# Kernel optimization log

Hardware: AMD Instinct MI355X
Metric: run time of the kernel (lower is better)

The kernel has to match this reference:

```python
import jax, jax.numpy as jnp
import numpy as np

B, N, H, E, WF = 2048, 30, 256, 256, 32
TANH_C = 10.0  # tanh_exploration


def _mask_modify(m):
    # if a row is all True, un-mask the last column
    all_true = jnp.all(m, axis=1)
    return m.at[:, -1].set(m[:, -1] & ~all_true)


def _lstm_cell(x, h, c, W_ih, W_hh, b_ih, b_hh):
    gates = x @ W_ih.T + b_ih + h @ W_hh.T + b_hh
    i, f, g, o = jnp.split(gates, 4, axis=1)  # torch LSTMCell gate order
    c_new = jax.nn.sigmoid(f) * c + jax.nn.sigmoid(i) * jnp.tanh(g)
    h_new = jax.nn.sigmoid(o) * jnp.tanh(c_new)
    return h_new, c_new


def _attention(query, ref, Wq, bq, Wr, br, v, C=None):
    # query [B,H], ref [B,H,N] (context permuted)
    q = query @ Wq.T + bq                                        # [B,H]
    e = jnp.einsum('oh,bhn->bon', Wr, ref) + br[None, :, None]   # 1x1 conv
    u = jnp.einsum('h,bhn->bn', v, jnp.tanh(q[:, :, None] + e))  # [B,N]
    logits = C * jnp.tanh(u) if C is not None else u
    return e, logits


def setup_inputs() -> dict:
    key = jax.random.key(0)
    ks = jax.random.split(key, 24)
    s = 0.06  # ~1/sqrt(H) init scale
    n = lambda k, sh: jax.random.normal(k, sh, dtype=jnp.float32)
    return {
        'decoder_input': n(ks[0], (B, E)),
        'embedded_inputs': n(ks[1], (N, B, E)),
        'h0': n(ks[2], (B, H)),
        'c0': n(ks[3], (B, H)),
        'context': n(ks[4], (N, B, H)),
        'embed_cou': n(ks[5], (B, WF)),
        'D': jax.random.uniform(ks[6], (B, N, N), dtype=jnp.float32),
        'W_ih': n(ks[7], (4 * H, E)) * s,
        'W_hh': n(ks[8], (4 * H, H)) * s,
        'b_ih': n(ks[9], (4 * H,)) * s,
        'b_hh': n(ks[10], (4 * H,)) * s,
        'W_merge': n(ks[11], (H, H + WF)) * s,
        'b_merge': n(ks[12], (H,)) * s,
        'Wq_p': n(ks[13], (H, H)) * s,
        'bq_p': n(ks[14], (H,)) * s,
        'Wr_p': n(ks[15], (H, H)) * s,
        'br_p': n(ks[16], (H,)) * s,
        'v_p': n(ks[17], (H,)) * s,
        'Wq_g': n(ks[18], (H, H)) * s,
        'bq_g': n(ks[19], (H,)) * s,
        'Wr_g': n(ks[20], (H, H)) * s,
        'br_g': n(ks[21], (H,)) * s,
        'v_g': n(ks[22], (H,)) * s,
        'V_reach_mask_t': jnp.zeros((B, N), dtype=bool),
        'start_idx': jax.random.randint(ks[23], (B,), 0, N),
        'k_min_nodes': 3,
    }


def reference(decoder_input, embedded_inputs, h0, c0, context, embed_cou, D,
              W_ih, W_hh, b_ih, b_hh, W_merge, b_merge,
              Wq_p, bq_p, Wr_p, br_p, v_p,
              Wq_g, bq_g, Wr_g, br_g, v_g,
              V_reach_mask_t, start_idx, k_min_nodes):
    ref = jnp.transpose(context, (1, 2, 0))  # [B,H,N]
    arangeB = jnp.arange(B)
    arangeN = jnp.arange(N)

    def step(carry, _):
        h, c, mask, idxs, dec_in, knn_row = carry
        # --- update_knn_mask ('n-1'): builds the row used at the NEXT step ---
        Eb = D[arangeB, idxs]                                  # [B,N]
        weighted = Eb * (~mask).astype(Eb.dtype)
        valid = jnp.sum(~mask, axis=1) > k_min_nodes
        far = jnp.argmax(weighted, axis=1)
        next_row = (arangeN[None, :] == far[:, None]) & valid[:, None]
        # --- recurrence: update_mask + check_mask ---
        lm = mask.at[arangeB, idxs].set(True)
        lm = _mask_modify(_mask_modify(lm))
        full_mask = lm | knn_row
        # LSTM step + worker-feature merge
        hy, cy = _lstm_cell(dec_in, h, c, W_ih, W_hh, b_ih, b_hh)
        g_l = jnp.concatenate([hy, embed_cou], axis=1) @ W_merge.T + b_merge
        # one glimpse (n_glimpses=1)
        e_g, lg = _attention(g_l, ref, Wq_g, bq_g, Wr_g, br_g, v_g)
        lg = jnp.where(full_mask, -jnp.inf, lg)
        g_l = jnp.einsum('bhn,bn->bh', e_g, jax.nn.softmax(lg, axis=1))
        # pointer (use_tanh with C)
        _, lp = _attention(g_l, ref, Wq_p, bq_p, Wr_p, br_p, v_p, C=TANH_C)
        lp = jnp.where(full_mask, -jnp.inf, lp)
        log_p = jax.nn.log_softmax(lp, axis=1)
        new_idxs = jnp.argmax(log_p, axis=1)  # greedy decode
        new_dec = embedded_inputs[new_idxs, arangeB]  # [B,E]
        return (hy, cy, lm, new_idxs, new_dec, next_row), (log_p, new_idxs)

    init = (h0, c0, V_reach_mask_t, start_idx, decoder_input,
            jnp.zeros_like(V_reach_mask_t))
    (_, _, mask, _, _, _), (logps, sels) = jax.lax.scan(step, init, None, length=N)
    return jnp.swapaxes(logps, 0, 1), jnp.swapaxes(sels, 0, 1), mask
```

## Files before the change

### kernel.cpp

```cpp
#include <hip/hip_runtime.h>
#include <hip/hip_bf16.h>
#include <math.h>

#define B 2048
#define NN 30
#define H 256
#define EDIM 256
#define G4 1024
#define PAD 44

typedef __attribute__((ext_vector_type(8))) short short8;
typedef __attribute__((ext_vector_type(4))) float f32x4;

__device__ __forceinline__ float fsig(float x) {
    return __fdividef(1.f, 1.f + __expf(-x));
}
__device__ __forceinline__ float ftanh(float x) {
    return 1.f - __fdividef(2.f, __expf(2.f * x) + 1.f);
}

__device__ __forceinline__ void split3(float a, unsigned short& h,
                                       unsigned short& m_, unsigned short& l_)
{
    unsigned ab = __float_as_uint(a);
    h = (unsigned short)(ab >> 16);
    float r1 = a - __uint_as_float(ab & 0xffff0000u);
    unsigned rb = __float_as_uint(r1);
    m_ = (unsigned short)(rb >> 16);
    float r2 = r1 - __uint_as_float(rb & 0xffff0000u);
    l_ = (unsigned short)(__float_as_uint(r2) >> 16);
}

__global__ __launch_bounds__(256)
void gemm_big(const float* __restrict__ A,
              const unsigned short* __restrict__ Wh, const unsigned short* __restrict__ Wm,
              const unsigned short* __restrict__ Wl,
              const float* __restrict__ b0, const float* __restrict__ b1,
              const float* __restrict__ b2,
              float* __restrict__ C0, float* __restrict__ C1,
              float* __restrict__ C2)
{
    __shared__ __align__(16) unsigned short Ah[128][PAD];
    __shared__ __align__(16) unsigned short Am[128][PAD];
    __shared__ __align__(16) unsigned short Al[128][PAD];
    __shared__ __align__(16) unsigned short Bh[128][PAD];
    __shared__ __align__(16) unsigned short Bm[128][PAD];
    __shared__ __align__(16) unsigned short Bl[128][PAD];

    int tid = threadIdx.x;
    int w = tid >> 6, l = tid & 63;

    int lin = blockIdx.y * 6 + blockIdx.x;
    int v = (lin & 7) * 360 + (lin >> 3);
    int m0 = (v / 6) << 7;
    int nblk = v % 6;
    int part = nblk >> 1;
    int nin = (nblk & 1) << 7;
    const float* bias = part == 0 ? b0 : part == 1 ? b1 : b2;
    float* C          = part == 0 ? C0 : part == 1 ? C1 : C2;
    long woff = (long)part * 65536;

    int srow = tid >> 1;
    int skb  = (tid & 1) << 4;
    const float* arow = A + (long)(m0 + srow) * 256 + skb;
    const unsigned short* wph = Wh + woff + (long)(nin + srow) * 256 + skb;
    const unsigned short* wpm = Wm + woff + (long)(nin + srow) * 256 + skb;
    const unsigned short* wpl = Wl + woff + (long)(nin + srow) * 256 + skb;

    int fr = l & 15;
    int fk = (l >> 4) << 3;

    f32x4 acc[2][8];
    #pragma unroll
    for (int i = 0; i < 2; ++i)
        #pragma unroll
        for (int j = 0; j < 8; ++j)
            acc[i][j] = (f32x4){0.f, 0.f, 0.f, 0.f};

    for (int kt = 0; kt < 8; ++kt) {
        int k0 = kt << 5;
        float4 a4[4];
        #pragma unroll
        for (int i = 0; i < 4; ++i)
            a4[i] = *(const float4*)(arow + k0 + (i << 2));
        short8 wh0 = *(const short8*)(wph + k0);
        short8 wh1 = *(const short8*)(wph + k0 + 8);
        short8 wm0 = *(const short8*)(wpm + k0);
        short8 wm1 = *(const short8*)(wpm + k0 + 8);
        short8 wl0 = *(const short8*)(wpl + k0);
        short8 wl1 = *(const short8*)(wpl + k0 + 8);

        unsigned short th[16], tm[16], tl[16];
        #pragma unroll
        for (int i = 0; i < 4; ++i) {
            float va[4] = {a4[i].x, a4[i].y, a4[i].z, a4[i].w};
            #pragma unroll
            for (int j = 0; j < 4; ++j)
                split3(va[j], th[(i << 2) + j], tm[(i << 2) + j], tl[(i << 2) + j]);
        }

        __syncthreads();
        *(short8*)&Ah[srow][skb]     = *(const short8*)&th[0];
        *(short8*)&Ah[srow][skb + 8] = *(const short8*)&th[8];
        *(short8*)&Am[srow][skb]     = *(const short8*)&tm[0];
        *(short8*)&Am[srow][skb + 8] = *(const short8*)&tm[8];
        *(short8*)&Al[srow][skb]     = *(const short8*)&tl[0];
        *(short8*)&Al[srow][skb + 8] = *(const short8*)&tl[8];
        *(short8*)&Bh[srow][skb]     = wh0;
        *(short8*)&Bh[srow][skb + 8] = wh1;
        *(short8*)&Bm[srow][skb]     = wm0;
        *(short8*)&Bm[srow][skb + 8] = wm1;
        *(short8*)&Bl[srow][skb]     = wl0;
        *(short8*)&Bl[srow][skb + 8] = wl1;
        __syncthreads();

        short8 aH[2], aM[2], aL[2];
        #pragma unroll
        for (int ms = 0; ms < 2; ++ms) {
            int r = (w << 5) + (ms << 4) + fr;
            aH[ms] = *(const short8*)&Ah[r][fk];
            aM[ms] = *(const short8*)&Am[r][fk];
            aL[ms] = *(const short8*)&Al[r][fk];
        }
        #pragma unroll
        for (int ng = 0; ng < 2; ++ng) {
            short8 bH[4], bM[4], bL[4];
            #pragma unroll
            for (int j = 0; j < 4; ++j) {
                int r = (((ng << 2) + j) << 4) + fr;
                bH[j] = *(const short8*)&Bh[r][fk];
                bM[j] = *(const short8*)&Bm[r][fk];
                bL[j] = *(const short8*)&Bl[r][fk];
            }
            #pragma unroll
            for (int ms = 0; ms < 2; ++ms)
                #pragma unroll
                for (int j = 0; j < 4; ++j)
                    acc[ms][(ng << 2) + j] = __builtin_amdgcn_mfma_f32_16x16x32_bf16(
                        aH[ms], bH[j], acc[ms][(ng << 2) + j], 0, 0, 0);
            #pragma unroll
            for (int ms = 0; ms < 2; ++ms)
                #pragma unroll
                for (int j = 0; j < 4; ++j)
                    acc[ms][(ng << 2) + j] = __builtin_amdgcn_mfma_f32_16x16x32_bf16(
                        aH[ms], bM[j], acc[ms][(ng << 2) + j], 0, 0, 0);
            #pragma unroll
            for (int ms = 0; ms < 2; ++ms)
                #pragma unroll
                for (int j = 0; j < 4; ++j)
                    acc[ms][(ng << 2) + j] = __builtin_amdgcn_mfma_f32_16x16x32_bf16(
                        aM[ms], bH[j], acc[ms][(ng << 2) + j], 0, 0, 0);
            #pragma unroll
            for (int ms = 0; ms < 2; ++ms)
                #pragma unroll
                for (int j = 0; j < 4; ++j)
                    acc[ms][(ng << 2) + j] = __builtin_amdgcn_mfma_f32_16x16x32_bf16(
                        aH[ms], bL[j], acc[ms][(ng << 2) + j], 0, 0, 0);
            #pragma unroll
            for (int ms = 0; ms < 2; ++ms)
                #pragma unroll
                for (int j = 0; j < 4; ++j)
                    acc[ms][(ng << 2) + j] = __builtin_amdgcn_mfma_f32_16x16x32_bf16(
                        aM[ms], bM[j], acc[ms][(ng << 2) + j], 0, 0, 0);
            #pragma unroll
            for (int ms = 0; ms < 2; ++ms)
                #pragma unroll
                for (int j = 0; j < 4; ++j)
                    acc[ms][(ng << 2) + j] = __builtin_amdgcn_mfma_f32_16x16x32_bf16(
                        aL[ms], bH[j], acc[ms][(ng << 2) + j], 0, 0, 0);
        }
    }

    #pragma unroll
    for (int ms = 0; ms < 2; ++ms) {
        #pragma unroll
        for (int ns = 0; ns < 8; ++ns) {
            float bv = bias[nin + (ns << 4) + fr];
            #pragma unroll
            for (int r = 0; r < 4; ++r) {
                int m = m0 + (w << 5) + (ms << 4) + ((l >> 4) << 2) + r;
                C[(long)m * 256 + nin + (ns << 4) + fr] = acc[ms][ns][r] + bv;
            }
        }
    }
}

__global__ __launch_bounds__(256)
void gates_mfma(const unsigned short* __restrict__ dhi, const unsigned short* __restrict__ dlo,
                const unsigned short* __restrict__ hhi, const unsigned short* __restrict__ hlo,
                const unsigned short* __restrict__ Whi, const unsigned short* __restrict__ Wlo,
                const float* __restrict__ bsum, const float* __restrict__ cin,
                float* __restrict__ hout, float* __restrict__ cout,
                unsigned short* __restrict__ hohi, unsigned short* __restrict__ holo)
{
    __shared__ __align__(16) unsigned short Ah[128][PAD];
    __shared__ __align__(16) unsigned short Al[128][PAD];
    __shared__ __align__(16) unsigned short Bh[64][PAD];
    __shared__ __align__(16) unsigned short Bl[64][PAD];

    int tid = threadIdx.x;
    int w = tid >> 6, l = tid & 63;
    int lin = blockIdx.x;
    int v = (lin & 7) * 32 + (lin >> 3);
    int m0 = (v >> 4) << 7;
    int u0 = (v & 15) << 4;

    int arow = tid >> 1;
    int akb  = (tid & 1) << 4;
    int brw  = tid >> 2;
    int bkb  = (tid & 3) << 3;
    int wrow = ((brw >> 4) << 8) + u0 + (brw & 15);
    const unsigned short* wph = Whi + (long)wrow * 512 + bkb;
    const unsigned short* wpl = Wlo + (long)wrow * 512 + bkb;

    int fk = (l >> 4) << 3;
    int fr = l & 15;

    f32x4 acc[2][4];
    #pragma unroll
    for (int i = 0; i < 2; ++i)
        #pragma unroll
        for (int j = 0; j < 4; ++j)
            acc[i][j] = (f32x4){0.f, 0.f, 0.f, 0.f};

    for (int kt = 0; kt < 16; ++kt) {
        int k0 = kt << 5;
        const unsigned short* sah; const unsigned short* sal; int kk;
        if (k0 < 256) { sah = dhi; sal = dlo; kk = k0; }
        else          { sah = hhi; sal = hlo; kk = k0 - 256; }
        long abase = (long)(m0 + arow) * 256 + kk + akb;
        short8 a0 = *(const short8*)&sah[abase];
        short8 a1 = *(const short8*)&sah[abase + 8];
        short8 a2 = *(const short8*)&sal[abase];
        short8 a3 = *(const short8*)&sal[abase + 8];
        short8 b0 = *(const short8*)&wph[k0];
        short8 b1 = *(const short8*)&wpl[k0];
        __syncthreads();
        *(short8*)&Ah[arow][akb]     = a0;
        *(short8*)&Ah[arow][akb + 8] = a1;
        *(short8*)&Al[arow][akb]     = a2;
        *(short8*)&Al[arow][akb + 8] = a3;
        *(short8*)&Bh[brw][bkb] = b0;
        *(short8*)&Bl[brw][bkb] = b1;
        __syncthreads();

        short8 aH[2], aL[2], bH[4], bL[4];
        #pragma unroll
        for (int ms = 0; ms < 2; ++ms) {
            int r = (w << 5) + (ms << 4) + fr;
            aH[ms] = *(const short8*)&Ah[r][fk];
            aL[ms] = *(const short8*)&Al[r][fk];
        }
        #pragma unroll
        for (int s = 0; s < 4; ++s) {
            int r = (s << 4) + fr;
            bH[s] = *(const short8*)&Bh[r][fk];
            bL[s] = *(const short8*)&Bl[r][fk];
        }
        #pragma unroll
        for (int ms = 0; ms < 2; ++ms)
            #pragma unroll
            for (int s = 0; s < 4; ++s)
                acc[ms][s] = __builtin_amdgcn_mfma_f32_16x16x32_bf16(aH[ms], bH[s], acc[ms][s], 0, 0, 0);
        #pragma unroll
        for (int ms = 0; ms < 2; ++ms)
            #pragma unroll
            for (int s = 0; s < 4; ++s)
                acc[ms][s] = __builtin_amdgcn_mfma_f32_16x16x32_bf16(aH[ms], bL[s], acc[ms][s], 0, 0, 0);
        #pragma unroll
        for (int ms = 0; ms < 2; ++ms)
            #pragma unroll
            for (int s = 0; s < 4; ++s)
                acc[ms][s] = __builtin_amdgcn_mfma_f32_16x16x32_bf16(aL[ms], bH[s], acc[ms][s], 0, 0, 0);
    }

    int u = u0 + fr;
    float bI = bsum[u], bF = bsum[256 + u], bG = bsum[512 + u], bO = bsum[768 + u];
    #pragma unroll
    for (int ms = 0; ms < 2; ++ms) {
        #pragma unroll
        for (int r = 0; r < 4; ++r) {
            int m = m0 + (w << 5) + (ms << 4) + ((l >> 4) << 2) + r;
            float gi = acc[ms][0][r] + bI;
            float gf = acc[ms][1][r] + bF;
            float gg = acc[ms][2][r] + bG;
            float go = acc[ms][3][r] + bO;
            float cv = cin[(long)m * H + u];
            float cn = fsig(gf) * cv + fsig(gi) * ftanh(gg);
            float hn = fsig(go) * ftanh(cn);
            cout[(long)m * H + u] = cn;
            hout[(long)m * H + u] = hn;
            unsigned hb = __float_as_uint(hn);
            hohi[(long)m * H + u] = (unsigned short)(hb >> 16);
            float lo = hn - __uint_as_float(hb & 0xffff0000u);
            holo[(long)m * H + u] = (unsigned short)(__float_as_uint(lo) >> 16);
        }
    }
}

__global__ void init_state(const unsigned char* __restrict__ vr, const int* __restrict__ start,
                           unsigned char* __restrict__ mask, unsigned char* __restrict__ knn,
                           int* __restrict__ idxs)
{
    int t = blockIdx.x * 256 + threadIdx.x;
    if (t < B * NN) { mask[t] = vr[t] ? 1 : 0; knn[t] = 0; }
    if (t < B) idxs[t] = start[t];
}

__global__ void prep_wsplit(const float* __restrict__ Wih, const float* __restrict__ Whh,
                            const float* __restrict__ bih, const float* __restrict__ bhh,
                            unsigned short* __restrict__ Whi, unsigned short* __restrict__ Wlo,
                            float* __restrict__ bsum)
{
    int n = blockIdx.x, k = threadIdx.x;
    float a = Wih[(long)n * H + k];
    unsigned ab = __float_as_uint(a);
    Whi[(long)n * 512 + k] = (unsigned short)(ab >> 16);
    float alo = a - __uint_as_float(ab & 0xffff0000u);
    Wlo[(long)n * 512 + k] = (unsigned short)(__float_as_uint(alo) >> 16);
    float b = Whh[(long)n * H + k];
    unsigned bb = __float_as_uint(b);
    Whi[(long)n * 512 + 256 + k] = (unsigned short)(bb >> 16);
    float blo = b - __uint_as_float(bb & 0xffff0000u);
    Wlo[(long)n * 512 + 256 + k] = (unsigned short)(__float_as_uint(blo) >> 16);
    if (k == 0) bsum[n] = bih[n] + bhh[n];
}

__global__ void prep_splitW(const float* __restrict__ W0, const float* __restrict__ W1,
                            const float* __restrict__ W2,
                            unsigned short* __restrict__ Wh, unsigned short* __restrict__ Wm,
                            unsigned short* __restrict__ Wl)
{
    int id = blockIdx.x;
    int p = id >> 8, r = id & 255, k = threadIdx.x;
    const float* W = p == 0 ? W0 : p == 1 ? W1 : W2;
    float a = W[(long)r * 256 + k];
    long o = (long)p * 65536 + (long)r * 256 + k;
    split3(a, Wh[o], Wm[o], Wl[o]);
}

__global__ void conv_pair(const float* __restrict__ x,
                          unsigned short* __restrict__ xhi, unsigned short* __restrict__ xlo)
{
    int t = blockIdx.x * 256 + threadIdx.x;
    float a = x[t];
    unsigned ab = __float_as_uint(a);
    xhi[t] = (unsigned short)(ab >> 16);
    float lo = a - __uint_as_float(ab & 0xffff0000u);
    xlo[t] = (unsigned short)(__float_as_uint(lo) >> 16);
}

__global__ void prep_compose1(const float* __restrict__ Wqg, const float* __restrict__ Wm,
                              float* __restrict__ W1cT)
{
    int h = blockIdx.x, k = threadIdx.x;
    float a = 0.f;
    for (int j = 0; j < H; ++j) a = fmaf(Wqg[(long)h * H + j], Wm[(long)j * 288 + k], a);
    W1cT[(long)k * H + h] = a;
}

__global__ void prep_compose2(const float* __restrict__ Wqg, const float* __restrict__ Wm,
                              const float* __restrict__ bm, const float* __restrict__ bqg,
                              float* __restrict__ W2c, float* __restrict__ bc)
{
    int h = blockIdx.x, w = threadIdx.x;
    if (w < 32) {
        float a = 0.f;
        for (int j = 0; j < H; ++j) a = fmaf(Wqg[(long)h * H + j], Wm[(long)j * 288 + 256 + w], a);
        W2c[h * 32 + w] = a;
    } else if (w == 32) {
        float a = 0.f;
        for (int j = 0; j < H; ++j) a = fmaf(Wqg[(long)h * H + j], bm[j], a);
        bc[h] = a + bqg[h];
    }
}

__global__ __launch_bounds__(256)
void prep_qc(const float* __restrict__ cou, const float* __restrict__ W2c,
             const float* __restrict__ bc, float* __restrict__ qc)
{
    __shared__ float sWT[32 * 256];
    __shared__ float sb[256];
    int b = blockIdx.x, h = threadIdx.x;
    for (int i = h; i < 32 * 256; i += 256) {
        int hh = i >> 5, ww = i & 31;
        sWT[ww * 256 + hh] = W2c[i];
    }
    sb[h] = bc[h];
    __syncthreads();
    const float* cr = cou + (long)b * 32;
    float a = sb[h];
    for (int w = 0; w < 32; ++w) a = fmaf(cr[w], sWT[w * 256 + h], a);
    qc[(long)b * H + h] = a;
}

__global__ void prep_composeF(const float* __restrict__ Wqp, const float* __restrict__ Wrg,
                              const float* __restrict__ brg, float* __restrict__ WFc,
                              float* __restrict__ bFc)
{
    int f = blockIdx.x, k = threadIdx.x;
    float a = 0.f;
    for (int j = 0; j < H; ++j) a = fmaf(Wqp[(long)f * H + j], Wrg[(long)j * H + k], a);
    WFc[(long)f * H + k] = a;
    if (k == 0) {
        float s = 0.f;
        for (int j = 0; j < H; ++j) s = fmaf(Wqp[(long)f * H + j], brg[j], s);
        bFc[f] = s;
    }
}

__global__ __launch_bounds__(512)
void mega8(const float* __restrict__ eg, const float* __restrict__ ep,
           const float* __restrict__ F, const float* __restrict__ hout,
           const float* __restrict__ qc, const float* __restrict__ W1cT,
           const float* __restrict__ vg, const float* __restrict__ vp,
           const float* __restrict__ bqp,
           const float* __restrict__ D, const int* __restrict__ kminp,
           unsigned char* __restrict__ mask, unsigned char* __restrict__ knn,
           const float* __restrict__ emb,
           float* __restrict__ out, int step,
           int* __restrict__ idxs,
           unsigned short* __restrict__ dechi, unsigned short* __restrict__ declo)
{
    __shared__ float sHy[4][256];
    __shared__ float sQg[4][256];
    __shared__ float sU[4][32];
    __shared__ float sPar[4][2][256];
    __shared__ unsigned char sFull[4][32];

    int tid = threadIdx.x;
    int wv = tid >> 6, lane = tid & 63;
    int pi = wv >> 1, sub = wv & 1;
    int blk = blockIdx.x;
    int vB = (blk & 7) * 64 + (blk >> 3);
    int b0 = vB << 2;
    int b = b0 + pi;

    #pragma unroll
    for (int i = 0; i < 2; ++i) {
        int idx2 = tid + (i << 9);
        int bl = idx2 >> 8, hh = idx2 & 255;
        sHy[bl][hh] = hout[(long)(b0 + bl) * H + hh];
    }
    __syncthreads();

    {
        int hh = tid & 255, g = tid >> 8;
        float a0 = 0.f, a1 = 0.f;
        const float* wp = W1cT + hh;
        const float* h0p = sHy[(g << 1)];
        const float* h1p = sHy[(g << 1) + 1];
        #pragma unroll 4
        for (int k = 0; k < 256; ++k) {
            float wval = wp[(long)k * H];
            a0 = fmaf(h0p[k], wval, a0);
            a1 = fmaf(h1p[k], wval, a1);
        }
        sQg[(g << 1)][hh]     = qc[(long)(b0 + (g << 1)) * H + hh] + a0;
        sQg[(g << 1) + 1][hh] = qc[(long)(b0 + (g << 1) + 1) * H + hh] + a1;
    }

    if (sub == 0) {
        bool in = lane < NN;
        int idx = idxs[b];
        int kmin = *kminp;
        unsigned char m = in ? mask[b * NN + lane] : (unsigned char)1;
        float dv = in ? D[((long)b * NN + idx) * NN + lane] : 0.f;
        unsigned long long unm = __ballot(in && !m);
        int cnt = __popcll(unm);
        bool valid = cnt > kmin;
        float bw = (in && !m) ? dv : (in ? 0.f : -1.f);
        int bi = in ? lane : 1000;
        #pragma unroll
        for (int off = 32; off; off >>= 1) {
            float ow = __shfl_down(bw, off, 64);
            int oi = __shfl_down(bi, off, 64);
            if (ow > bw || (ow == bw && oi < bi)) { bw = ow; bi = oi; }
        }
        int far = __shfl(bi, 0, 64);
        unsigned char mnew = (in && lane == idx) ? 1 : m;
        #pragma unroll
        for (int rep = 0; rep < 2; ++rep) {
            bool allm = (__ballot(in && !mnew) == 0ull);
            if (allm && lane == NN - 1) mnew = 0;
        }
        unsigned char kn = in ? knn[b * NN + lane] : 0;
        if (in) {
            sFull[pi][lane] = (mnew | kn) ? 1 : 0;
            mask[b * NN + lane] = mnew;
            knn[b * NN + lane] = (lane == far && valid) ? 1 : 0;
        }
    }
    __syncthreads();

    float4 vg4 = ((const float4*)vg)[lane];
    float4 vp4 = ((const float4*)vp)[lane];

    {
        float4 q4 = ((const float4*)&sQg[pi][0])[lane];
        for (int n = sub; n < NN; n += 2) {
            if (sFull[pi][n]) continue;
            float4 e4 = ((const float4*)(eg + ((long)n * B + b) * H))[lane];
            float s = vg4.x * ftanh(q4.x + e4.x);
            s = fmaf(vg4.y, ftanh(q4.y + e4.y), s);
            s = fmaf(vg4.z, ftanh(q4.z + e4.z), s);
            s = fmaf(vg4.w, ftanh(q4.w + e4.w), s);
            #pragma unroll
            for (int off = 32; off; off >>= 1) s += __shfl_down(s, off, 64);
            if (lane == 0) sU[pi][n] = s;
        }
    }
    __syncthreads();

    float pr;
    {
        bool in = lane < NN;
        bool fm = in ? (sFull[pi][lane] != 0) : true;
        float u = (in && !fm) ? sU[pi][lane] : -INFINITY;
        float mx = u;
        #pragma unroll
        for (int off = 32; off; off >>= 1) mx = fmaxf(mx, __shfl_down(mx, off, 64));
        mx = __shfl(mx, 0, 64);
        float p = (in && !fm) ? __expf(u - mx) : 0.f;
        float sum = p;
        #pragma unroll
        for (int off = 32; off; off >>= 1) sum += __shfl_down(sum, off, 64);
        sum = __shfl(sum, 0, 64);
        pr = p / sum;
    }

    {
        float4 qa = {0.f, 0.f, 0.f, 0.f};
        for (int n = sub; n < NN; n += 2) {
            float pn = __shfl(pr, n, 64);
            if (pn != 0.f) {
                float4 F4 = ((const float4*)(F + ((long)n * B + b) * H))[lane];
                qa.x = fmaf(pn, F4.x, qa.x);
                qa.y = fmaf(pn, F4.y, qa.y);
                qa.z = fmaf(pn, F4.z, qa.z);
                qa.w = fmaf(pn, F4.w, qa.w);
            }
        }
        ((float4*)&sPar[pi][sub][0])[lane] = qa;
    }
    __syncthreads();

    float4 qp4;
    {
        float4 p0 = ((const float4*)&sPar[pi][0][0])[lane];
        float4 p1 = ((const float4*)&sPar[pi][1][0])[lane];
        float4 bq4 = ((const float4*)bqp)[lane];
        qp4 = make_float4(bq4.x + p0.x + p1.x, bq4.y + p0.y + p1.y,
                          bq4.z + p0.z + p1.z, bq4.w + p0.w + p1.w);
    }

    for (int n = sub; n < NN; n += 2) {
        if (sFull[pi][n]) continue;
        float4 e4 = ((const float4*)(ep + ((long)n * B + b) * H))[lane];
        float s = vp4.x * ftanh(qp4.x + e4.x);
        s = fmaf(vp4.y, ftanh(qp4.y + e4.y), s);
        s = fmaf(vp4.z, ftanh(qp4.z + e4.z), s);
        s = fmaf(vp4.w, ftanh(qp4.w + e4.w), s);
        #pragma unroll
        for (int off = 32; off; off >>= 1) s += __shfl_down(s, off, 64);
        if (lane == 0) sU[pi][n] = 10.f * ftanh(s);
    }
    __syncthreads();

    {
        bool in = lane < NN;
        bool fm = in ? (sFull[pi][lane] != 0) : true;
        float lg = (in && !fm) ? sU[pi][lane] : -INFINITY;
        float mx = lg; int bi = in ? lane : 1000;
        #pragma unroll
        for (int off = 32; off; off >>= 1) {
            float om = __shfl_down(mx, off, 64);
            int oi = __shfl_down(bi, off, 64);
            if (om > mx || (om == mx && oi < bi)) { mx = om; bi = oi; }
        }
        mx = __shfl(mx, 0, 64);
        bi = __shfl(bi, 0, 64);
        float pe = (in && !fm) ? __expf(lg - mx) : 0.f;
        float sum = pe;
        #pragma unroll
        for (int off = 32; off; off >>= 1) sum += __shfl_down(sum, off, 64);
        sum = __shfl(sum, 0, 64);
        float lse = mx + __logf(sum);
        if (sub == 0) {
            if (lane == 0) {
                idxs[b] = bi;
                out[(long)B * NN * NN + (long)b * NN + step] = (float)bi;
            }
            if (in)
                out[(long)b * NN * NN + (long)step * NN + lane] =
                    fm ? -1e30f : (lg - lse);
        }
        int sel = bi;
        int hbase = lane + (sub ? 128 : 0);
        #pragma unroll
        for (int j = 0; j < 2; ++j) {
            int hh = hbase + (j << 6);
            float d = emb[((long)sel * B + b) * EDIM + hh];
            unsigned db = __float_as_uint(d);
            dechi[(long)b * H + hh] = (unsigned short)(db >> 16);
            float lo = d - __uint_as_float(db & 0xffff0000u);
            declo[(long)b * H + hh] = (unsigned short)(__float_as_uint(lo) >> 16);
        }
    }
}

__global__ void mask_out(const unsigned char* __restrict__ mask, float* __restrict__ out)
{
    int t = blockIdx.x * 256 + threadIdx.x;
    if (t < B * NN)
        out[(long)B * NN * NN + (long)B * NN + t] = mask[t] ? 1.f : 0.f;
}

extern "C" void kernel_launch(void* const* d_in, const int* in_sizes, int n_in,
                              void* d_out, int out_size, void* d_ws, size_t ws_size,
                              hipStream_t stream)
{
    const float* decoder_input = (const float*)d_in[0];
    const float* embedded     = (const float*)d_in[1];
    const float* h0           = (const float*)d_in[2];
    const float* c0           = (const float*)d_in[3];
    const float* context      = (const float*)d_in[4];
    const float* embed_cou    = (const float*)d_in[5];
    const float* D            = (const float*)d_in[6];
    const float* W_ih         = (const float*)d_in[7];
    const float* W_hh         = (const float*)d_in[8];
    const float* b_ih         = (const float*)d_in[9];
    const float* b_hh         = (const float*)d_in[10];
    const float* W_merge      = (const float*)d_in[11];
    const float* b_merge      = (const float*)d_in[12];
    const float* Wq_p         = (const float*)d_in[13];
    const float* bq_p         = (const float*)d_in[14];
    const float* Wr_p         = (const float*)d_in[15];
    const float* br_p         = (const float*)d_in[16];
    const float* v_p          = (const float*)d_in[17];
    const float* Wq_g         = (const float*)d_in[18];
    const float* bq_g         = (const float*)d_in[19];
    const float* Wr_g         = (const float*)d_in[20];
    const float* br_g         = (const float*)d_in[21];
    const float* v_g          = (const float*)d_in[22];
    const unsigned char* vreach = (const unsigned char*)d_in[23];
    const int* start_idx      = (const int*)d_in[24];
    const int* kminp          = (const int*)d_in[25];

    float* ws = (float*)d_ws;
    size_t o = 0;
    float* eg     = ws + o; o += (size_t)B * NN * H;
    float* ep     = ws + o; o += (size_t)B * NN * H;
    float* Fbuf   = ws + o; o += (size_t)B * NN * H;
    float* hb0    = ws + o; o += (size_t)B * H;
    float* hb1    = ws + o; o += (size_t)B * H;
    float* cb0    = ws + o; o += (size_t)B * H;
    float* cb1    = ws + o; o += (size_t)B * H;
    float* qc     = ws + o; o += (size_t)B * H;
    float* W1cT   = ws + o; o += (size_t)H * H;
    float* W2c    = ws + o; o += (size_t)H * 32;
    float* bc     = ws + o; o += (size_t)H;
    float* WFc    = ws + o; o += (size_t)H * H;
    float* bFc    = ws + o; o += (size_t)H;
    float* bsum   = ws + o; o += (size_t)G4;
    unsigned short* Whi  = (unsigned short*)(ws + o); o += (size_t)G4 * 512 / 2;
    unsigned short* Wlo  = (unsigned short*)(ws + o); o += (size_t)G4 * 512 / 2;
    unsigned short* Wsh  = (unsigned short*)(ws + o); o += (size_t)3 * 65536 / 2;
    unsigned short* Wsm  = (unsigned short*)(ws + o); o += (size_t)3 * 65536 / 2;
    unsigned short* Wsl  = (unsigned short*)(ws + o); o += (size_t)3 * 65536 / 2;
    unsigned short* dechi = (unsigned short*)(ws + o); o += (size_t)B * H / 2;
    unsigned short* declo = (unsigned short*)(ws + o); o += (size_t)B * H / 2;
    unsigned short* hAhi = (unsigned short*)(ws + o); o += (size_t)B * H / 2;
    unsigned short* hAlo = (unsigned short*)(ws + o); o += (size_t)B * H / 2;
    unsigned short* hBhi = (unsigned short*)(ws + o); o += (size_t)B * H / 2;
    unsigned short* hBlo = (unsigned short*)(ws + o); o += (size_t)B * H / 2;
    unsigned char* maskb = (unsigned char*)(ws + o);
    unsigned char* knnb  = maskb + (size_t)B * NN;
    int* idxs = (int*)(knnb + (size_t)B * NN + 64);

    float* out = (float*)d_out;

    init_state<<<dim3((B * NN + 255) / 256), dim3(256), 0, stream>>>(
        vreach, start_idx, maskb, knnb, idxs);

    prep_wsplit<<<dim3(G4), dim3(256), 0, stream>>>(W_ih, W_hh, b_ih, b_hh,
                                                    Whi, Wlo, bsum);
    conv_pair<<<dim3(B * H / 256), dim3(256), 0, stream>>>(decoder_input, dechi, declo);
    conv_pair<<<dim3(B * H / 256), dim3(256), 0, stream>>>(h0, hAhi, hAlo);
    prep_compose1<<<dim3(H), dim3(256), 0, stream>>>(Wq_g, W_merge, W1cT);
    prep_compose2<<<dim3(H), dim3(64), 0, stream>>>(Wq_g, W_merge, b_merge, bq_g,
                                                    W2c, bc);
    prep_qc<<<dim3(B), dim3(256), 0, stream>>>(embed_cou, W2c, bc, qc);
    prep_composeF<<<dim3(H), dim3(256), 0, stream>>>(Wq_p, Wr_g, br_g, WFc, bFc);
    prep_splitW<<<dim3(3 * 256), dim3(256), 0, stream>>>(Wr_g, Wr_p, WFc,
                                                         Wsh, Wsm, Wsl);

    gemm_big<<<dim3(6, (B * NN) / 128), dim3(256), 0, stream>>>(
        context, Wsh, Wsm, Wsl, br_g, br_p, bFc, eg, ep, Fbuf);

    const float* cin = c0;
    unsigned short* hInHi = hAhi; unsigned short* hInLo = hAlo;
    unsigned short* hOutHi = hBhi; unsigned short* hOutLo = hBlo;

    for (int step = 0; step < NN; ++step) {
        int p = step & 1;
        float* hout = p ? hb1 : hb0;
        float* cout = p ? cb1 : cb0;

        gates_mfma<<<dim3(256), dim3(256), 0, stream>>>(
            dechi, declo, hInHi, hInLo, Whi, Wlo, bsum, cin,
            hout, cout, hOutHi, hOutLo);

        mega8<<<dim3(B / 4), dim3(512), 0, stream>>>(
            eg, ep, Fbuf, hout, qc, W1cT, v_g, v_p, bq_p, D, kminp,
            maskb, knnb, embedded, out, step, idxs, dechi, declo);

        cin = cout;
        unsigned short* th = hInHi; hInHi = hOutHi; hOutHi = th;
        unsigned short* tl = hInLo; hInLo = hOutLo; hOutLo = tl;
    }

    mask_out<<<dim3((B * NN + 255) / 256), dim3(256), 0, stream>>>(maskb, out);
}
```

Before: 2.192 ms.

## Prefetch next K-tile global loads into registers during MFMA in GEMM kernels

Both split-precision GEMM loops now issue the global loads for the next K tile right after the LDS store barrier, so they overlap with the current tile's LDS reads and MFMA work instead of stalling at the top of each iteration. The LDS row padding also changes from 44 to 40 elements. This costs extra live registers, which may lower occupancy, and the new padding may alter LDS bank conflict patterns.

```diff
diff --git a/kernel.cpp b/kernel.cpp
--- a/kernel.cpp
+++ b/kernel.cpp
@@ -7,7 +7,7 @@
 #define H 256
 #define EDIM 256
 #define G4 1024
-#define PAD 44
+#define PAD 40
 
 typedef __attribute__((ext_vector_type(8))) short short8;
 typedef __attribute__((ext_vector_type(4))) float f32x4;
@@ -77,19 +77,19 @@
         for (int j = 0; j < 8; ++j)
             acc[i][j] = (f32x4){0.f, 0.f, 0.f, 0.f};
 
+    float4 a4[4];
+    short8 wh0, wh1, wm0, wm1, wl0, wl1;
+    #pragma unroll
+    for (int i = 0; i < 4; ++i)
+        a4[i] = *(const float4*)(arow + (i << 2));
+    wh0 = *(const short8*)(wph);
+    wh1 = *(const short8*)(wph + 8);
+    wm0 = *(const short8*)(wpm);
+    wm1 = *(const short8*)(wpm + 8);
+    wl0 = *(const short8*)(wpl);
+    wl1 = *(const short8*)(wpl + 8);
+
     for (int kt = 0; kt < 8; ++kt) {
-        int k0 = kt << 5;
-        float4 a4[4];
-        #pragma unroll
-        for (int i = 0; i < 4; ++i)
-            a4[i] = *(const float4*)(arow + k0 + (i << 2));
-        short8 wh0 = *(const short8*)(wph + k0);
-        short8 wh1 = *(const short8*)(wph + k0 + 8);
-        short8 wm0 = *(const short8*)(wpm + k0);
-        short8 wm1 = *(const short8*)(wpm + k0 + 8);
-        short8 wl0 = *(const short8*)(wpl + k0);
-        short8 wl1 = *(const short8*)(wpl + k0 + 8);
-
         unsigned short th[16], tm[16], tl[16];
         #pragma unroll
         for (int i = 0; i < 4; ++i) {
@@ -114,6 +114,19 @@
         *(short8*)&Bl[srow][skb + 8] = wl1;
         __syncthreads();
 
+        if (kt + 1 < 8) {
+            int k1 = (kt + 1) << 5;
+            #pragma unroll
+            for (int i = 0; i < 4; ++i)
+                a4[i] = *(const float4*)(arow + k1 + (i << 2));
+            wh0 = *(const short8*)(wph + k1);
+            wh1 = *(const short8*)(wph + k1 + 8);
+            wm0 = *(const short8*)(wpm + k1);
+            wm1 = *(const short8*)(wpm + k1 + 8);
+            wl0 = *(const short8*)(wpl + k1);
+            wl1 = *(const short8*)(wpl + k1 + 8);
+        }
+
         short8 aH[2], aM[2], aL[2];
         #pragma unroll
         for (int ms = 0; ms < 2; ++ms) {
@@ -223,18 +236,18 @@
         for (int j = 0; j < 4; ++j)
             acc[i][j] = (f32x4){0.f, 0.f, 0.f, 0.f};
 
+    short8 a0, a1, a2, a3, b0, b1;
+    {
+        long abase = (long)(m0 + arow) * 256 + akb;
+        a0 = *(const short8*)&dhi[abase];
+        a1 = *(const short8*)&dhi[abase + 8];
+        a2 = *(const short8*)&dlo[abase];
+        a3 = *(const short8*)&dlo[abase + 8];
+        b0 = *(const short8*)&wph[0];
+        b1 = *(const short8*)&wpl[0];
+    }
+
     for (int kt = 0; kt < 16; ++kt) {
-        int k0 = kt << 5;
-        const unsigned short* sah; const unsigned short* sal; int kk;
-        if (k0 < 256) { sah = dhi; sal = dlo; kk = k0; }
-        else          { sah = hhi; sal = hlo; kk = k0 - 256; }
-        long abase = (long)(m0 + arow) * 256 + kk + akb;
-        short8 a0 = *(const short8*)&sah[abase];
-        short8 a1 = *(const short8*)&sah[abase + 8];
-        short8 a2 = *(const short8*)&sal[abase];
-        short8 a3 = *(const short8*)&sal[abase + 8];
-        short8 b0 = *(const short8*)&wph[k0];
-        short8 b1 = *(const short8*)&wpl[k0];
         __syncthreads();
         *(short8*)&Ah[arow][akb]     = a0;
         *(short8*)&Ah[arow][akb + 8] = a1;
@@ -243,6 +256,20 @@
         *(short8*)&Bh[brw][bkb] = b0;
         *(short8*)&Bl[brw][bkb] = b1;
         __syncthreads();
+
+        if (kt + 1 < 16) {
+            int k1 = (kt + 1) << 5;
+            const unsigned short* sah; const unsigned short* sal; int kk;
+            if (k1 < 256) { sah = dhi; sal = dlo; kk = k1; }
+            else          { sah = hhi; sal = hlo; kk = k1 - 256; }
+            long abase = (long)(m0 + arow) * 256 + kk + akb;
+            a0 = *(const short8*)&sah[abase];
+            a1 = *(const short8*)&sah[abase + 8];
+            a2 = *(const short8*)&sal[abase];
+            a3 = *(const short8*)&sal[abase + 8];
+            b0 = *(const short8*)&wph[k1];
+            b1 = *(const short8*)&wpl[k1];
+        }
 
         short8 aH[2], aL[2], bH[4], bL[4];
         #pragma unroll
```

After: 2.177 ms (median of 2 runs). About the same (-0.7%).
